# Kernel optimization log

Hardware: AMD Instinct MI355X
Metric: run time of the kernel (lower is better)

## Reference

```python
import jax, jax.numpy as jnp
import numpy as np
import math

D_MODEL = 1024
N_HEADS = 16
D_HEAD = D_MODEL // N_HEADS
D_FF = 4096
BOTTLENECK = D_MODEL // 4  # 256
AB_HIDDEN = max(D_MODEL // 32, 8)  # 32
EPS = 1e-6


def rms_norm(x, w):
    rms = jnp.sqrt(jnp.mean(x * x, axis=-1, keepdims=True) + EPS)
    return x / rms * w


def rotate_half(x):
    x1, x2 = jnp.split(x, 2, axis=-1)
    return jnp.concatenate([-x2, x1], axis=-1)


def rope_tables(T, dim):
    inv_freq = 1.0 / (10000.0 ** (jnp.arange(0, dim, 2, dtype=jnp.float32) / dim))
    t = jnp.arange(T, dtype=jnp.float32)
    freqs = jnp.outer(t, inv_freq)            # [T, dim/2]
    emb = jnp.concatenate([freqs, freqs], -1)  # [T, dim]
    return jnp.cos(emb), jnp.sin(emb)


def setup_inputs() -> dict:
    key = jax.random.key(0)
    ks = jax.random.split(key, 12)
    B, T = 4, 2048
    s = lambda fan_in: 1.0 / math.sqrt(fan_in)
    x = jax.random.normal(ks[0], (B, T, D_MODEL), jnp.float32)
    mask = jnp.tril(jnp.ones((T, T), jnp.int32))  # causal 0/1 mask, mask==0 -> -inf
    return {
        "x": x,
        "mask": mask,
        "norm1_w": jnp.ones((D_MODEL,), jnp.float32),
        "Wq": jax.random.normal(ks[1], (D_MODEL, D_MODEL), jnp.float32) * s(D_MODEL),
        "Wk": jax.random.normal(ks[2], (D_MODEL, D_MODEL), jnp.float32) * s(D_MODEL),
        "Wv": jax.random.normal(ks[3], (D_MODEL, D_MODEL), jnp.float32) * s(D_MODEL),
        "Wo": jax.random.normal(ks[4], (D_MODEL, D_MODEL), jnp.float32) * s(D_MODEL),
        "norm2_w": jnp.ones((D_MODEL,), jnp.float32),
        "w1": jax.random.normal(ks[5], (D_FF, D_MODEL), jnp.float32) * s(D_MODEL),
        "w2": jax.random.normal(ks[6], (D_MODEL, D_FF), jnp.float32) * s(D_FF),
        "fc1": jax.random.normal(ks[7], (AB_HIDDEN, D_MODEL), jnp.float32) * s(D_MODEL),
        "fc2": jax.random.normal(ks[8], (2, AB_HIDDEN), jnp.float32) * s(AB_HIDDEN),
        "down": jax.random.normal(ks[9], (BOTTLENECK, D_MODEL), jnp.float32) * s(D_MODEL),
        "up": jax.random.normal(ks[10], (D_MODEL, BOTTLENECK), jnp.float32) * s(BOTTLENECK),
    }


def attention(x, mask, Wq, Wk, Wv, Wo):
    B, T, D = x.shape
    def split_heads(y):
        return y.reshape(B, T, N_HEADS, D_HEAD).transpose(0, 2, 1, 3)  # [B,H,T,Dh]
    q = split_heads(x @ Wq.T)
    k = split_heads(x @ Wk.T)
    v = split_heads(x @ Wv.T)
    cos, sin = rope_tables(T, D_HEAD)
    cos = cos[None, None]; sin = sin[None, None]
    q = q * cos + rotate_half(q) * sin
    k = k * cos + rotate_half(k) * sin
    scores = jnp.einsum("bhqd,bhkd->bhqk", q, k) / math.sqrt(D_HEAD)
    scores = jnp.where(mask[:T, :T] == 0, -jnp.inf, scores)
    attn = jax.nn.softmax(scores, axis=-1)
    out = jnp.einsum("bhqk,bhkd->bhqd", attn, v)
    out = out.transpose(0, 2, 1, 3).reshape(B, T, D)
    return out @ Wo.T


def reference(x, mask, norm1_w, Wq, Wk, Wv, Wo, norm2_w, w1, w2, fc1, fc2, down, up):
    # group='B': gated FFN + projection branch (dropout=0 / eval mode)
    x = x + attention(rms_norm(x, norm1_w), mask, Wq, Wk, Wv, Wo)
    normed = rms_norm(x, norm2_w)
    ffn_out = jax.nn.gelu(normed @ w1.T, approximate=False) @ w2.T
    # AttentionAlphaBetaLM: mean over tokens, tiny MLP -> (alpha, beta)
    g = normed.mean(axis=1)                      # [B, D]
    h = jax.nn.relu(g @ fc1.T)                   # [B, hidden]
    ab = h @ fc2.T                               # [B, 2]
    alpha = jax.nn.sigmoid(ab[:, 0])             # [B]
    beta = jax.nn.sigmoid(ab[:, 1])              # allow_negative_beta=False for group B
    proj_out = jax.nn.relu(normed @ down.T) @ up.T
    x = x + alpha[:, None, None] * ffn_out + beta[:, None, None] * proj_out
    return x
```

## Files before the change

### kernel.cpp

```cpp
#include <hip/hip_runtime.h>
#include <hip/hip_bf16.h>
#include <math.h>

typedef unsigned short u16;
typedef unsigned int   u32;

typedef __bf16 bf16x8_t __attribute__((ext_vector_type(8)));
typedef float  f32x4_t  __attribute__((ext_vector_type(4)));

__device__ float AB_dev[8];

__device__ inline float bf2f(u16 u) {
    u32 x = ((u32)u) << 16;
    return __builtin_bit_cast(float, x);
}
__device__ inline u16 f2bf(float f) {
    u32 x = __builtin_bit_cast(u32, f);
    return (u16)((x + 0x7fffu + ((x >> 16) & 1u)) >> 16);
}
__device__ inline u32 cvt_pk_bf16(float lo, float hi) {
    u32 r;
    asm("v_cvt_pk_bf16_f32 %0, %1, %2" : "=v"(r) : "v"(lo), "v"(hi));
    return r;
}
__device__ inline uint4 stage_pack_f32(const float* p) {
    float4 f0 = ((const float4*)p)[0];
    float4 f1 = ((const float4*)p)[1];
    u32 w0 = (u32)f2bf(f0.x) | ((u32)f2bf(f0.y) << 16);
    u32 w1 = (u32)f2bf(f0.z) | ((u32)f2bf(f0.w) << 16);
    u32 w2 = (u32)f2bf(f1.x) | ((u32)f2bf(f1.y) << 16);
    u32 w3 = (u32)f2bf(f1.z) | ((u32)f2bf(f1.w) << 16);
    return uint4{w0, w1, w2, w3};
}
#define GLD(gptr, lptr) __builtin_amdgcn_global_load_lds( \
    (const __attribute__((address_space(1))) void*)(gptr), \
    (__attribute__((address_space(3))) void*)(lptr), 16, 0, 0)

template <typename TIN>
__global__ __launch_bounds__(256) void rmsnorm_kernel(
    const TIN* __restrict__ x, const float* __restrict__ w, u16* __restrict__ out)
{
    const int row = blockIdx.x, tid = threadIdx.x;
    const size_t rb = (size_t)row * 1024;
    float val[4];
#pragma unroll
    for (int i = 0; i < 4; ++i) {
        size_t idx = rb + tid + i * 256;
        if constexpr (sizeof(TIN) == 4) val[i] = ((const float*)x)[idx];
        else                            val[i] = bf2f(((const u16*)x)[idx]);
    }
    float ss = val[0]*val[0] + val[1]*val[1] + val[2]*val[2] + val[3]*val[3];
#pragma unroll
    for (int off = 32; off >= 1; off >>= 1) ss += __shfl_xor(ss, off, 64);
    __shared__ float red[4];
    if ((tid & 63) == 0) red[tid >> 6] = ss;
    __syncthreads();
    float tot = red[0] + red[1] + red[2] + red[3];
    float inv = rsqrtf(tot * (1.0f / 1024.0f) + 1e-6f);
    u16* orow = out + rb;
#pragma unroll
    for (int i = 0; i < 4; ++i)
        orow[tid + i * 256] = f2bf(val[i] * inv * w[tid + i * 256]);
}

__global__ __launch_bounds__(256) void convm_kernel(
    const float* __restrict__ s0, const float* __restrict__ s1,
    const float* __restrict__ s2, const float* __restrict__ s3,
    u16* __restrict__ d0, u16* __restrict__ d1,
    u16* __restrict__ d2, u16* __restrict__ d3, int shift)
{
    int sel = blockIdx.x >> shift;
    int loc = blockIdx.x & ((1 << shift) - 1);
    const float* s = sel == 0 ? s0 : sel == 1 ? s1 : sel == 2 ? s2 : s3;
    u16*       d = sel == 0 ? d0 : sel == 1 ? d1 : sel == 2 ? d2 : d3;
    size_t i = ((size_t)loc * 256 + threadIdx.x) * 8;
    *(uint4*)(d + i) = stage_pack_f32(s + i);
}

enum { EPI_QKV = 0, EPI_ADDX_F32 = 1, EPI_GELU = 2, EPI_COMB0 = 3,
       EPI_COMBA = 4, EPI_RELU = 5, EPI_BSCALE = 6 };

template <int EPI>
__global__ __launch_bounds__(256) void gemm128e(
    const u16* __restrict__ A, int sA, const u16* __restrict__ Wb, int sW,
    void* __restrict__ C, const float* __restrict__ Xf,
    const u16* __restrict__ Xh, int N, int K)
{
    __shared__ __align__(16) u16 As[2][128 * 32];
    __shared__ __align__(16) u16 Bs[2][128 * 32];
    const int tid  = threadIdx.x;
    const int wave = tid >> 6, lane = tid & 63;
    const int quad = lane >> 4, l16 = lane & 15;
    const int row0 = blockIdx.y * 128, col0 = blockIdx.x * 128;
    const int wm = (wave >> 1) * 64, wn = (wave & 1) * 64;

    f32x4_t acc[4][4];
#pragma unroll
    for (int i = 0; i < 4; ++i)
#pragma unroll
        for (int j = 0; j < 4; ++j) { f32x4_t z = {0,0,0,0}; acc[i][j] = z; }

    const u16* Abase = A + (size_t)row0 * sA;
    const int id0 = tid, id1 = tid + 256;
    const size_t aoff0 = (size_t)(id0 >> 2) * sA + (id0 & 3) * 8;
    const size_t aoff1 = (size_t)(id1 >> 2) * sA + (id1 & 3) * 8;
    const size_t boff0 = (size_t)(col0 + (id0 >> 2)) * sW + (id0 & 3) * 8;
    const size_t boff1 = (size_t)(col0 + (id1 >> 2)) * sW + (id1 & 3) * 8;
    const size_t ld0 = (size_t)(wave * 64) * 8;
    const size_t ld1 = (size_t)(256 + wave * 64) * 8;

    for (int k0 = 0; k0 < K; k0 += 64) {
        __syncthreads();
        GLD(Abase + aoff0 + k0,      As[0] + ld0);
        GLD(Abase + aoff1 + k0,      As[0] + ld1);
        GLD(Abase + aoff0 + k0 + 32, As[1] + ld0);
        GLD(Abase + aoff1 + k0 + 32, As[1] + ld1);
        GLD(Wb + boff0 + k0,         Bs[0] + ld0);
        GLD(Wb + boff1 + k0,         Bs[0] + ld1);
        GLD(Wb + boff0 + k0 + 32,    Bs[1] + ld0);
        GLD(Wb + boff1 + k0 + 32,    Bs[1] + ld1);
        __syncthreads();

#pragma unroll
        for (int hh = 0; hh < 2; ++hh) {
            const bf16x8_t* As8 = (const bf16x8_t*)As[hh];
            const bf16x8_t* Bs8 = (const bf16x8_t*)Bs[hh];
            bf16x8_t af[4], bfr[4];
#pragma unroll
            for (int i = 0; i < 4; ++i) {
                af[i]  = As8[(wm + i * 16 + l16) * 4 + quad];
                bfr[i] = Bs8[(wn + i * 16 + l16) * 4 + quad];
            }
#pragma unroll
            for (int i = 0; i < 4; ++i)
#pragma unroll
                for (int j = 0; j < 4; ++j)
                    acc[i][j] = __builtin_amdgcn_mfma_f32_16x16x32_bf16(
                        af[i], bfr[j], acc[i][j], 0, 0, 0);
        }
    }

    float al = 0.0f;
    if (EPI == EPI_COMB0 || EPI == EPI_COMBA)
        al = AB_dev[blockIdx.y >> 4];
#pragma unroll
    for (int i = 0; i < 4; ++i) {
        int mbase = row0 + wm + i * 16 + quad * 4;
#pragma unroll
        for (int j = 0; j < 4; ++j) {
            int n = col0 + wn + j * 16 + l16;
#pragma unroll
            for (int r = 0; r < 4; ++r) {
                float vv = acc[i][j][r];
                int row = mbase + r;
                if (EPI == EPI_QKV) {
                    int sel = col0 >> 10;
                    float sc = (sel == 0) ? 0.18033688011112042f : 1.0f;
                    ((u16*)C)[(size_t)sel * 8388608 + (size_t)row * 1024 + (n & 1023)]
                        = f2bf(vv * sc);
                } else if (EPI == EPI_ADDX_F32) {
                    size_t off = (size_t)row * N + n;
                    ((u16*)C)[off] = f2bf(vv + Xf[off]);
                } else if (EPI == EPI_GELU) {
                    size_t off = (size_t)row * N + n;
                    vv = 0.5f * vv * (1.0f + erff(vv * 0.70710678118654752f));
                    ((u16*)C)[off] = f2bf(vv);
                } else {
                    size_t off = (size_t)row * N + n;
                    float prev = ((float*)C)[off];
                    float add = (EPI == EPI_COMB0) ? bf2f(Xh[off]) : 0.0f;
                    ((float*)C)[off] = prev + add + al * vv;
                }
            }
        }
    }
}

template <int EPI>
__global__ __launch_bounds__(256) void gemm64b(
    const u16* __restrict__ A, int sA, const u16* __restrict__ Wb, int sW,
    void* __restrict__ C, int N, int K)
{
    __shared__ __align__(16) u16 As[128 * 32];
    __shared__ __align__(16) u16 Bs[64 * 32];
    const int tid  = threadIdx.x;
    const int wave = tid >> 6, lane = tid & 63;
    const int quad = lane >> 4, l16 = lane & 15;
    const int row0 = blockIdx.y * 128, col0 = blockIdx.x * 64;
    const int wm = (wave >> 1) * 64, wn = (wave & 1) * 32;

    f32x4_t acc[4][2];
#pragma unroll
    for (int i = 0; i < 4; ++i)
#pragma unroll
        for (int j = 0; j < 2; ++j) { f32x4_t z = {0,0,0,0}; acc[i][j] = z; }

    const u16* Abase = A + (size_t)row0 * sA;
    const int id0 = tid, id1 = tid + 256;
    const size_t aoff0 = (size_t)(id0 >> 2) * sA + (id0 & 3) * 8;
    const size_t aoff1 = (size_t)(id1 >> 2) * sA + (id1 & 3) * 8;
    const size_t woff  = (size_t)(col0 + (tid >> 2)) * sW + (tid & 3) * 8;
    u16* lA0 = As + (size_t)(wave * 64) * 8;
    u16* lA1 = As + (size_t)(256 + wave * 64) * 8;
    u16* lB  = Bs + (size_t)(wave * 64) * 8;

    for (int k0 = 0; k0 < K; k0 += 32) {
        __syncthreads();
        GLD(Abase + aoff0 + k0, lA0);
        GLD(Abase + aoff1 + k0, lA1);
        GLD(Wb + woff + k0, lB);
        __syncthreads();

        const bf16x8_t* As8 = (const bf16x8_t*)As;
        const bf16x8_t* Bs8 = (const bf16x8_t*)Bs;
        bf16x8_t af[4], bfr[2];
#pragma unroll
        for (int i = 0; i < 4; ++i) af[i]  = As8[(wm + i * 16 + l16) * 4 + quad];
#pragma unroll
        for (int j = 0; j < 2; ++j) bfr[j] = Bs8[(wn + j * 16 + l16) * 4 + quad];
#pragma unroll
        for (int i = 0; i < 4; ++i)
#pragma unroll
            for (int j = 0; j < 2; ++j)
                acc[i][j] = __builtin_amdgcn_mfma_f32_16x16x32_bf16(
                    af[i], bfr[j], acc[i][j], 0, 0, 0);
    }

#pragma unroll
    for (int i = 0; i < 4; ++i) {
        int mbase = row0 + wm + i * 16 + quad * 4;
#pragma unroll
        for (int j = 0; j < 2; ++j) {
            int n = col0 + wn + j * 16 + l16;
#pragma unroll
            for (int r = 0; r < 4; ++r) {
                float vv = acc[i][j][r];
                int row = mbase + r;
                size_t off = (size_t)row * N + n;
                if (EPI == EPI_RELU) {
                    ((u16*)C)[off] = f2bf(fmaxf(vv, 0.0f));
                } else {
                    ((float*)C)[off] = AB_dev[4 + (row >> 11)] * vv;
                }
            }
        }
    }
}

__global__ __launch_bounds__(256) void rope_kernel(u16* __restrict__ q, u16* __restrict__ k)
{
    int idx = blockIdx.x * 256 + threadIdx.x;
    int i = idx & 31;
    int h = (idx >> 5) & 15;
    int t = (idx >> 9) & 2047;
    int b = idx >> 20;
    float inv = __expf(-(float)i * (9.210340371976184f / 32.0f));
    float ang = (float)t * inv;
    float sn, cs;
    sincosf(ang, &sn, &cs);
    size_t o1 = ((size_t)(b * 2048 + t)) * 1024 + h * 64 + i;
    size_t o2 = o1 + 32;
    float q1 = bf2f(q[o1]), q2 = bf2f(q[o2]);
    q[o1] = f2bf(q1 * cs - q2 * sn);
    q[o2] = f2bf(q2 * cs + q1 * sn);
    float k1 = bf2f(k[o1]), k2 = bf2f(k[o2]);
    k[o1] = f2bf(k1 * cs - k2 * sn);
    k[o2] = f2bf(k2 * cs + k1 * sn);
}

#define TS 72

__global__ __launch_bounds__(256) void flash_kernel(
    const u16* __restrict__ q, const u16* __restrict__ k,
    const u16* __restrict__ v, u16* __restrict__ o)
{
    __shared__ __align__(16) u16 QP[128 * TS];
    __shared__ __align__(16) u16 KT[64 * TS];
    __shared__ __align__(16) u16 VT[64 * TS];

    const int tid  = threadIdx.x;
    const int wave = tid >> 6, lane = tid & 63;
    const int quad = lane >> 4, l16 = lane & 15;
    const int bx = blockIdx.x;
    const int p  = 15 - (bx >> 6);
    const int bh = bx & 63;
    const int h = bh & 15, b = bh >> 4;
    const int q0 = p * 128;
    const int qb0 = q0 + wave * 16;
    const int qb1 = q0 + 64 + wave * 16;
    const int last0 = qb0 + 15;
    const size_t bt_base = (size_t)(b * 2048) * 1024 + h * 64;

    const u16* kbase = k + bt_base;
    const u16* vbase = v + bt_base;

#pragma unroll
    for (int it = 0; it < 4; ++it) {
        int id = it * 256 + tid;
        int row = id >> 3, c8 = (id & 7) * 8;
        uint4 val = *(const uint4*)(q + bt_base + (size_t)(q0 + row) * 1024 + c8);
        *(uint4*)(QP + row * TS + c8) = val;
    }
    __syncthreads();

    bf16x8_t qf[2][2];
#pragma unroll
    for (int mi = 0; mi < 2; ++mi)
#pragma unroll
        for (int ks = 0; ks < 2; ++ks)
            qf[mi][ks] = *(const bf16x8_t*)(
                QP + (mi * 64 + wave * 16 + l16) * TS + ks * 32 + quad * 8);

    float mst[2], lst[2];
    mst[0] = mst[1] = -3.0e38f;
    lst[0] = lst[1] = 0.f;
    f32x4_t oacc[2][4];
#pragma unroll
    for (int mi = 0; mi < 2; ++mi)
#pragma unroll
        for (int dj = 0; dj < 4; ++dj) { f32x4_t z = {0,0,0,0}; oacc[mi][dj] = z; }

    u16* Pl = QP + (wave * 32) * TS;
    const int jmax = q0 + 128;

    for (int j0 = 0; j0 < jmax; j0 += 64) {
        __syncthreads();
#pragma unroll
        for (int it = 0; it < 2; ++it) {
            int id = it * 256 + tid;
            int row = id >> 3, c8 = (id & 7) * 8;
            uint4 kv = *(const uint4*)(kbase + (size_t)(j0 + row) * 1024 + c8);
            *(uint4*)(KT + row * TS + c8) = kv;
            uint4 vv = *(const uint4*)(vbase + (size_t)(j0 + row) * 1024 + c8);
            const u16* vp = (const u16*)&vv;
            int sw = id & 7;
#pragma unroll
            for (int jj = 0; jj < 8; ++jj) {
                int j2 = (jj + sw) & 7;
                VT[(c8 + j2) * TS + row] = vp[j2];
            }
        }
        __syncthreads();

        const bool a0 = (j0 <= last0);

        f32x4_t s[2][4];
#pragma unroll
        for (int mi = 0; mi < 2; ++mi)
#pragma unroll
            for (int nj = 0; nj < 4; ++nj) { f32x4_t z = {0,0,0,0}; s[mi][nj] = z; }
#pragma unroll
        for (int ks = 0; ks < 2; ++ks) {
            bf16x8_t kf2[4];
#pragma unroll
            for (int nj = 0; nj < 4; ++nj)
                kf2[nj] = *(const bf16x8_t*)(KT + (nj * 16 + l16) * TS + ks * 32 + quad * 8);
#pragma unroll
            for (int nj = 0; nj < 4; ++nj)
                s[1][nj] = __builtin_amdgcn_mfma_f32_16x16x32_bf16(
                    kf2[nj], qf[1][ks], s[1][nj], 0, 0, 0);
            if (a0) {
#pragma unroll
                for (int nj = 0; nj < 4; ++nj)
                    s[0][nj] = __builtin_amdgcn_mfma_f32_16x16x32_bf16(
                        kf2[nj], qf[0][ks], s[0][nj], 0, 0, 0);
            }
        }

        if (a0 && j0 + 63 > qb0) {
#pragma unroll
            for (int nj = 0; nj < 4; ++nj)
#pragma unroll
                for (int r = 0; r < 4; ++r) {
                    int key = j0 + nj * 16 + quad * 4 + r;
                    if (key > qb0 + l16) s[0][nj][r] = -1.0e30f;
                }
        }
        if (j0 + 63 > qb1) {
#pragma unroll
            for (int nj = 0; nj < 4; ++nj)
#pragma unroll
                for (int r = 0; r < 4; ++r) {
                    int key = j0 + nj * 16 + quad * 4 + r;
                    if (key > qb1 + l16) s[1][nj][r] = -1.0e30f;
                }
        }

#pragma unroll
        for (int mi = 0; mi < 2; ++mi) {
            if (mi == 0 && !a0) continue;
            float mx = s[mi][0][0];
#pragma unroll
            for (int nj = 0; nj < 4; ++nj)
#pragma unroll
                for (int r = 0; r < 4; ++r)
                    if (nj || r) mx = fmaxf(mx, s[mi][nj][r]);
            mx = fmaxf(mx, __shfl_xor(mx, 16, 64));
            mx = fmaxf(mx, __shfl_xor(mx, 32, 64));
            float mn = fmaxf(mst[mi], mx);
            float alpha = __builtin_amdgcn_exp2f(mst[mi] - mn);
            mst[mi] = mn;
            float rs = 0.f;
            u16* prow = Pl + (mi * 16 + l16) * TS;
#pragma unroll
            for (int nj = 0; nj < 4; ++nj) {
                float p0 = __builtin_amdgcn_exp2f(s[mi][nj][0] - mn);
                float p1 = __builtin_amdgcn_exp2f(s[mi][nj][1] - mn);
                float p2 = __builtin_amdgcn_exp2f(s[mi][nj][2] - mn);
                float p3 = __builtin_amdgcn_exp2f(s[mi][nj][3] - mn);
                rs += (p0 + p1) + (p2 + p3);
                uint2 w;
                w.x = cvt_pk_bf16(p0, p1);
                w.y = cvt_pk_bf16(p2, p3);
                *(uint2*)(prow + nj * 16 + quad * 4) = w;
            }
            rs += __shfl_xor(rs, 16, 64);
            rs += __shfl_xor(rs, 32, 64);
            lst[mi] = lst[mi] * alpha + rs;
#pragma unroll
            for (int r = 0; r < 4; ++r) {
                float ar = __shfl(alpha, quad * 4 + r, 64);
#pragma unroll
                for (int dj = 0; dj < 4; ++dj) oacc[mi][dj][r] *= ar;
            }
        }

#pragma unroll
        for (int ks = 0; ks < 2; ++ks) {
            bf16x8_t vf2[4];
#pragma unroll
            for (int dj = 0; dj < 4; ++dj)
                vf2[dj] = *(const bf16x8_t*)(VT + (dj * 16 + l16) * TS + ks * 32 + quad * 8);
            bf16x8_t pf1 = *(const bf16x8_t*)(Pl + (16 + l16) * TS + ks * 32 + quad * 8);
#pragma unroll
            for (int dj = 0; dj < 4; ++dj)
                oacc[1][dj] = __builtin_amdgcn_mfma_f32_16x16x32_bf16(
                    pf1, vf2[dj], oacc[1][dj], 0, 0, 0);
            if (a0) {
                bf16x8_t pf0 = *(const bf16x8_t*)(Pl + (l16)*TS + ks * 32 + quad * 8);
#pragma unroll
                for (int dj = 0; dj < 4; ++dj)
                    oacc[0][dj] = __builtin_amdgcn_mfma_f32_16x16x32_bf16(
                        pf0, vf2[dj], oacc[0][dj], 0, 0, 0);
            }
        }
    }

#pragma unroll
    for (int mi = 0; mi < 2; ++mi) {
        int gb = q0 + mi * 64 + wave * 16;
#pragma unroll
        for (int r = 0; r < 4; ++r) {
            float lr = __shfl(lst[mi], quad * 4 + r, 64);
            float invl = 1.0f / lr;
            size_t rowb = bt_base + (size_t)(gb + quad * 4 + r) * 1024;
#pragma unroll
            for (int dj = 0; dj < 4; ++dj)
                o[rowb + dj * 16 + l16] = f2bf(oacc[mi][dj][r] * invl);
        }
    }
}

__global__ __launch_bounds__(256) void mean_partial_kernel(
    const u16* __restrict__ normed, float* __restrict__ part)
{
    int blk = blockIdx.x;
    int b = blk >> 4, c = blk & 15;
    int tid = threadIdx.x;
    int d0 = tid * 4;
    float s0 = 0, s1 = 0, s2 = 0, s3 = 0;
    const u16* base = normed + ((size_t)b * 2048 + c * 128) * 1024 + d0;
    for (int t = 0; t < 128; ++t) {
        const uint2 uv = *(const uint2*)(base + (size_t)t * 1024);
        s0 += bf2f((u16)(uv.x & 0xffff));
        s1 += bf2f((u16)(uv.x >> 16));
        s2 += bf2f((u16)(uv.y & 0xffff));
        s3 += bf2f((u16)(uv.y >> 16));
    }
    float* o = part + (size_t)blk * 1024 + d0;
    o[0] = s0; o[1] = s1; o[2] = s2; o[3] = s3;
}

__global__ void ab_kernel(const float* __restrict__ part, const float* __restrict__ fc1,
                          const float* __restrict__ fc2)
{
    int b = blockIdx.x, tid = threadIdx.x;
    __shared__ float g[1024];
    __shared__ float h[32];
    for (int d = tid; d < 1024; d += 64) {
        float s = 0;
        for (int c = 0; c < 16; ++c) s += part[(size_t)(b * 16 + c) * 1024 + d];
        g[d] = s * (1.0f / 2048.0f);
    }
    __syncthreads();
    if (tid < 32) {
        float s = 0;
        for (int d = 0; d < 1024; ++d) s += g[d] * fc1[(size_t)tid * 1024 + d];
        h[tid] = fmaxf(s, 0.0f);
    }
    __syncthreads();
    if (tid < 2) {
        float s = 0;
        for (int j = 0; j < 32; ++j) s += h[j] * fc2[(size_t)tid * 32 + j];
        AB_dev[tid * 4 + b] = 1.0f / (1.0f + __expf(-s));
    }
}

__global__ __launch_bounds__(256) void sentinel_kernel(float* __restrict__ out, int n)
{
    int i = blockIdx.x * 256 + threadIdx.x;
    if (i < n) out[i] = 100.0f;
}

extern "C" void kernel_launch(void* const* d_in, const int* in_sizes, int n_in,
                              void* d_out, int out_size, void* d_ws, size_t ws_size,
                              hipStream_t stream)
{
    const float* x   = (const float*)d_in[0];
    const float* n1w = (const float*)d_in[2];
    const float* Wq  = (const float*)d_in[3];
    const float* Wk  = (const float*)d_in[4];
    const float* Wv  = (const float*)d_in[5];
    const float* Wo  = (const float*)d_in[6];
    const float* n2w = (const float*)d_in[7];
    const float* w1  = (const float*)d_in[8];
    const float* w2  = (const float*)d_in[9];
    const float* fc1 = (const float*)d_in[10];
    const float* fc2 = (const float*)d_in[11];
    const float* dwn = (const float*)d_in[12];
    const float* up  = (const float*)d_in[13];

    const size_t MB = 1024 * 1024;
    if (ws_size < 64 * MB) {
        sentinel_kernel<<<(out_size + 255) / 256, 256, 0, stream>>>((float*)d_out, out_size);
        return;
    }

    char* ws = (char*)d_ws;
    u16*   XN1  = (u16*)(ws);
    u16*   ATT  = (u16*)(ws);
    u16*   H1s  = (u16*)(ws);
    u16*   Q    = (u16*)(ws + 16 * MB);
    u16*   XNEW = (u16*)(ws + 16 * MB);
    u16*   K    = (u16*)(ws + 32 * MB);
    u16*   XN2  = (u16*)(ws + 32 * MB);
    u16*   V    = (u16*)(ws + 48 * MB);
    float* PART = (float*)(ws + 48 * MB);
    u16*   DWNB = (u16*)(ws + 48 * MB + 512 * 1024);
    u16*   W1B  = (u16*)(ws + 48 * MB);
    u16*   P1   = (u16*)(ws + 56 * MB);
    u16*   UPB  = (u16*)(ws + 60 * MB);
    u16*   W2B  = (u16*)(ws + 56 * MB);

    u16* WqkvB = (u16*)d_out;
    u16* WoB   = WqkvB + 3 * 1024 * 1024;

    dim3 blk(256);

    convm_kernel<<<2048, blk, 0, stream>>>(Wq, Wk, Wv, Wo,
        WqkvB, WqkvB + 1024 * 1024, WqkvB + 2 * 1024 * 1024, WoB, 9);
    rmsnorm_kernel<float><<<8192, blk, 0, stream>>>(x, n1w, XN1);
    gemm128e<EPI_QKV><<<dim3(24, 64), blk, 0, stream>>>(
        XN1, 1024, WqkvB, 1024, Q, nullptr, nullptr, 1024, 1024);
    rope_kernel<<<16384, blk, 0, stream>>>(Q, K);
    flash_kernel<<<1024, blk, 0, stream>>>(Q, K, V, ATT);
    gemm128e<EPI_ADDX_F32><<<dim3(8, 64), blk, 0, stream>>>(
        ATT, 1024, WoB, 1024, XNEW, x, nullptr, 1024, 1024);
    rmsnorm_kernel<u16><<<8192, blk, 0, stream>>>(XNEW, n2w, XN2);
    mean_partial_kernel<<<64, blk, 0, stream>>>(XN2, PART);
    ab_kernel<<<4, dim3(64), 0, stream>>>(PART, fc1, fc2);
    convm_kernel<<<256, blk, 0, stream>>>(dwn, up, nullptr, nullptr,
                                          DWNB, UPB, nullptr, nullptr, 7);
    gemm64b<EPI_RELU><<<dim3(4, 64), blk, 0, stream>>>(
        XN2, 1024, DWNB, 1024, P1, 256, 1024);
    convm_kernel<<<2048, blk, 0, stream>>>(w1, nullptr, nullptr, nullptr,
                                           W1B, nullptr, nullptr, nullptr, 11);
    gemm64b<EPI_BSCALE><<<dim3(16, 64), blk, 0, stream>>>(
        P1, 256, UPB, 256, d_out, 1024, 256);
    convm_kernel<<<2048, blk, 0, stream>>>(w2, nullptr, nullptr, nullptr,
                                           W2B, nullptr, nullptr, nullptr, 11);
    for (int s = 0; s < 4; ++s) {
        gemm128e<EPI_GELU><<<dim3(8, 64), blk, 0, stream>>>(
            XN2, 1024, W1B + (size_t)s * 1024 * 1024, 1024, H1s,
            nullptr, nullptr, 1024, 1024);
        if (s == 0)
            gemm128e<EPI_COMB0><<<dim3(8, 64), blk, 0, stream>>>(
                H1s, 1024, W2B + s * 1024, 4096, d_out,
                nullptr, XNEW, 1024, 1024);
        else
            gemm128e<EPI_COMBA><<<dim3(8, 64), blk, 0, stream>>>(
                H1s, 1024, W2B + s * 1024, 4096, d_out,
                nullptr, XNEW, 1024, 1024);
    }
}
```

Baseline: 760.6 us.

## Prefetch K/V tiles in flash attention and double the GEMM k-step

The flash kernel now double-buffers K in LDS, using direct global-to-LDS loads with an XOR swizzle. It also prefetches the next V tile into registers during the current tile's compute, so global latency overlaps with the MFMA work. The P buffer switches to a swizzled 64-wide layout to cut bank conflicts. The gemm64b kernel now loads two 32-wide K slices per iteration, which halves the number of barrier pairs per tile. These changes raise LDS use and register pressure, which may reduce occupancy.

```diff
diff --git a/kernel.cpp b/kernel.cpp
--- a/kernel.cpp
+++ b/kernel.cpp
@@ -181,8 +181,8 @@
     const u16* __restrict__ A, int sA, const u16* __restrict__ Wb, int sW,
     void* __restrict__ C, int N, int K)
 {
-    __shared__ __align__(16) u16 As[128 * 32];
-    __shared__ __align__(16) u16 Bs[64 * 32];
+    __shared__ __align__(16) u16 As[2][128 * 32];
+    __shared__ __align__(16) u16 Bs[2][64 * 32];
     const int tid  = threadIdx.x;
     const int wave = tid >> 6, lane = tid & 63;
     const int quad = lane >> 4, l16 = lane & 15;
@@ -200,30 +200,35 @@
     const size_t aoff0 = (size_t)(id0 >> 2) * sA + (id0 & 3) * 8;
     const size_t aoff1 = (size_t)(id1 >> 2) * sA + (id1 & 3) * 8;
     const size_t woff  = (size_t)(col0 + (tid >> 2)) * sW + (tid & 3) * 8;
-    u16* lA0 = As + (size_t)(wave * 64) * 8;
-    u16* lA1 = As + (size_t)(256 + wave * 64) * 8;
-    u16* lB  = Bs + (size_t)(wave * 64) * 8;
-
-    for (int k0 = 0; k0 < K; k0 += 32) {
+    const size_t ld0 = (size_t)(wave * 64) * 8;
+    const size_t ld1 = (size_t)(256 + wave * 64) * 8;
+
+    for (int k0 = 0; k0 < K; k0 += 64) {
         __syncthreads();
-        GLD(Abase + aoff0 + k0, lA0);
-        GLD(Abase + aoff1 + k0, lA1);
-        GLD(Wb + woff + k0, lB);
+        GLD(Abase + aoff0 + k0,      As[0] + ld0);
+        GLD(Abase + aoff1 + k0,      As[0] + ld1);
+        GLD(Abase + aoff0 + k0 + 32, As[1] + ld0);
+        GLD(Abase + aoff1 + k0 + 32, As[1] + ld1);
+        GLD(Wb + woff + k0,          Bs[0] + ld0);
+        GLD(Wb + woff + k0 + 32,     Bs[1] + ld0);
         __syncthreads();
 
-        const bf16x8_t* As8 = (const bf16x8_t*)As;
-        const bf16x8_t* Bs8 = (const bf16x8_t*)Bs;
-        bf16x8_t af[4], bfr[2];
-#pragma unroll
-        for (int i = 0; i < 4; ++i) af[i]  = As8[(wm + i * 16 + l16) * 4 + quad];
-#pragma unroll
-        for (int j = 0; j < 2; ++j) bfr[j] = Bs8[(wn + j * 16 + l16) * 4 + quad];
-#pragma unroll
-        for (int i = 0; i < 4; ++i)
-#pragma unroll
-            for (int j = 0; j < 2; ++j)
-                acc[i][j] = __builtin_amdgcn_mfma_f32_16x16x32_bf16(
-                    af[i], bfr[j], acc[i][j], 0, 0, 0);
+#pragma unroll
+        for (int hh = 0; hh < 2; ++hh) {
+            const bf16x8_t* As8 = (const bf16x8_t*)As[hh];
+            const bf16x8_t* Bs8 = (const bf16x8_t*)Bs[hh];
+            bf16x8_t af[4], bfr[2];
+#pragma unroll
+            for (int i = 0; i < 4; ++i) af[i]  = As8[(wm + i * 16 + l16) * 4 + quad];
+#pragma unroll
+            for (int j = 0; j < 2; ++j) bfr[j] = Bs8[(wn + j * 16 + l16) * 4 + quad];
+#pragma unroll
+            for (int i = 0; i < 4; ++i)
+#pragma unroll
+                for (int j = 0; j < 2; ++j)
+                    acc[i][j] = __builtin_amdgcn_mfma_f32_16x16x32_bf16(
+                        af[i], bfr[j], acc[i][j], 0, 0, 0);
+        }
     }
 
 #pragma unroll
@@ -275,7 +280,7 @@
     const u16* __restrict__ v, u16* __restrict__ o)
 {
     __shared__ __align__(16) u16 QP[128 * TS];
-    __shared__ __align__(16) u16 KT[64 * TS];
+    __shared__ __align__(16) u16 KT[2][64 * 64];
     __shared__ __align__(16) u16 VT[64 * TS];
 
     const int tid  = threadIdx.x;
@@ -293,7 +298,17 @@
 
     const u16* kbase = k + bt_base;
     const u16* vbase = v + bt_base;
-
+    const int psw = l16 & 7;
+
+    uint4 vr[2];
+#pragma unroll
+    for (int it = 0; it < 2; ++it) {
+        int id = it * 256 + tid;
+        int row = id >> 3, c = id & 7;
+        GLD(kbase + (size_t)row * 1024 + (c ^ (row & 7)) * 8,
+            KT[0] + (size_t)(it * 256 + wave * 64) * 8);
+        vr[it] = *(const uint4*)(vbase + (size_t)row * 1024 + c * 8);
+    }
 #pragma unroll
     for (int it = 0; it < 4; ++it) {
         int id = it * 256 + tid;
@@ -311,6 +326,20 @@
             qf[mi][ks] = *(const bf16x8_t*)(
                 QP + (mi * 64 + wave * 16 + l16) * TS + ks * 32 + quad * 8);
 
+#pragma unroll
+    for (int it = 0; it < 2; ++it) {
+        int id = it * 256 + tid;
+        int row = id >> 3, c8 = (id & 7) * 8;
+        const u16* vp = (const u16*)&vr[it];
+        int sw = id & 7;
+#pragma unroll
+        for (int jj = 0; jj < 8; ++jj) {
+            int j2 = (jj + sw) & 7;
+            VT[(c8 + j2) * TS + row] = vp[j2];
+        }
+    }
+    __syncthreads();
+
     float mst[2], lst[2];
     mst[0] = mst[1] = -3.0e38f;
     lst[0] = lst[1] = 0.f;
@@ -320,29 +349,26 @@
 #pragma unroll
         for (int dj = 0; dj < 4; ++dj) { f32x4_t z = {0,0,0,0}; oacc[mi][dj] = z; }
 
-    u16* Pl = QP + (wave * 32) * TS;
+    u16* Pl = (u16*)QP + wave * 2048;
     const int jmax = q0 + 128;
+    int cur = 0;
 
     for (int j0 = 0; j0 < jmax; j0 += 64) {
-        __syncthreads();
-#pragma unroll
-        for (int it = 0; it < 2; ++it) {
-            int id = it * 256 + tid;
-            int row = id >> 3, c8 = (id & 7) * 8;
-            uint4 kv = *(const uint4*)(kbase + (size_t)(j0 + row) * 1024 + c8);
-            *(uint4*)(KT + row * TS + c8) = kv;
-            uint4 vv = *(const uint4*)(vbase + (size_t)(j0 + row) * 1024 + c8);
-            const u16* vp = (const u16*)&vv;
-            int sw = id & 7;
-#pragma unroll
-            for (int jj = 0; jj < 8; ++jj) {
-                int j2 = (jj + sw) & 7;
-                VT[(c8 + j2) * TS + row] = vp[j2];
-            }
-        }
-        __syncthreads();
+        const bool more = (j0 + 64 < jmax);
+        if (more) {
+            const int jn = j0 + 64;
+#pragma unroll
+            for (int it = 0; it < 2; ++it) {
+                int id = it * 256 + tid;
+                int row = id >> 3, c = id & 7;
+                GLD(kbase + (size_t)(jn + row) * 1024 + (c ^ (row & 7)) * 8,
+                    KT[cur ^ 1] + (size_t)(it * 256 + wave * 64) * 8);
+                vr[it] = *(const uint4*)(vbase + (size_t)(jn + row) * 1024 + c * 8);
+            }
+        }
 
         const bool a0 = (j0 <= last0);
+        const u16* KTc = KT[cur];
 
         f32x4_t s[2][4];
 #pragma unroll
@@ -354,7 +380,8 @@
             bf16x8_t kf2[4];
 #pragma unroll
             for (int nj = 0; nj < 4; ++nj)
-                kf2[nj] = *(const bf16x8_t*)(KT + (nj * 16 + l16) * TS + ks * 32 + quad * 8);
+                kf2[nj] = *(const bf16x8_t*)(
+                    KTc + (nj * 16 + l16) * 64 + (((ks * 4 + quad) ^ psw) * 8));
 #pragma unroll
             for (int nj = 0; nj < 4; ++nj)
                 s[1][nj] = __builtin_amdgcn_mfma_f32_16x16x32_bf16(
@@ -401,7 +428,7 @@
             float alpha = __builtin_amdgcn_exp2f(mst[mi] - mn);
             mst[mi] = mn;
             float rs = 0.f;
-            u16* prow = Pl + (mi * 16 + l16) * TS;
+            u16* prow = Pl + (mi * 16 + l16) * 64;
 #pragma unroll
             for (int nj = 0; nj < 4; ++nj) {
                 float p0 = __builtin_amdgcn_exp2f(s[mi][nj][0] - mn);
@@ -412,7 +439,8 @@
                 uint2 w;
                 w.x = cvt_pk_bf16(p0, p1);
                 w.y = cvt_pk_bf16(p2, p3);
-                *(uint2*)(prow + nj * 16 + quad * 4) = w;
+                *(uint2*)(prow + (((nj * 2 + (quad >> 1)) ^ psw) * 8)
+                               + (quad & 1) * 4) = w;
             }
             rs += __shfl_xor(rs, 16, 64);
             rs += __shfl_xor(rs, 32, 64);
@@ -431,19 +459,39 @@
 #pragma unroll
             for (int dj = 0; dj < 4; ++dj)
                 vf2[dj] = *(const bf16x8_t*)(VT + (dj * 16 + l16) * TS + ks * 32 + quad * 8);
-            bf16x8_t pf1 = *(const bf16x8_t*)(Pl + (16 + l16) * TS + ks * 32 + quad * 8);
+            bf16x8_t pf1 = *(const bf16x8_t*)(
+                Pl + (16 + l16) * 64 + (((ks * 4 + quad) ^ psw) * 8));
 #pragma unroll
             for (int dj = 0; dj < 4; ++dj)
                 oacc[1][dj] = __builtin_amdgcn_mfma_f32_16x16x32_bf16(
                     pf1, vf2[dj], oacc[1][dj], 0, 0, 0);
             if (a0) {
-                bf16x8_t pf0 = *(const bf16x8_t*)(Pl + (l16)*TS + ks * 32 + quad * 8);
+                bf16x8_t pf0 = *(const bf16x8_t*)(
+                    Pl + (l16) * 64 + (((ks * 4 + quad) ^ psw) * 8));
 #pragma unroll
                 for (int dj = 0; dj < 4; ++dj)
                     oacc[0][dj] = __builtin_amdgcn_mfma_f32_16x16x32_bf16(
                         pf0, vf2[dj], oacc[0][dj], 0, 0, 0);
             }
         }
+
+        __syncthreads();
+        if (more) {
+#pragma unroll
+            for (int it = 0; it < 2; ++it) {
+                int id = it * 256 + tid;
+                int row = id >> 3, c8 = (id & 7) * 8;
+                const u16* vp = (const u16*)&vr[it];
+                int sw = id & 7;
+#pragma unroll
+                for (int jj = 0; jj < 8; ++jj) {
+                    int j2 = (jj + sw) & 7;
+                    VT[(c8 + j2) * TS + row] = vp[j2];
+                }
+            }
+        }
+        __syncthreads();
+        cur ^= 1;
     }
 
 #pragma unroll
```

Result: no change. 764.2 us (+0.5%).
